# Kernel optimization log

Hardware: AMD Instinct MI355X
Metric: run time of the kernel (lower is better)

## Reference

```python
import jax, jax.numpy as jnp
import numpy as np

B, T, IDIM, HDIM = 16, 512, 80, 512
TEMPER = 10.0


def _windows(key_pad, n_shifts, win):
    idx = jnp.arange(n_shifts)[:, None] + jnp.arange(win)[None, :]
    return key_pad[..., idx]


def setup_inputs() -> dict:
    key = jax.random.key(0)
    k1, k2, k3 = jax.random.split(key, 3)
    x = jax.random.normal(k1, (B, T, IDIM), dtype=jnp.float32)
    y = jax.random.normal(k2, (B, T, IDIM), dtype=jnp.float32)
    # xavier-uniform fc1 weight, zero bias (per initialize())
    limit = float(np.sqrt(6.0 / (IDIM + HDIM)))
    fc1_w = jax.random.uniform(k3, (HDIM, IDIM), jnp.float32, -limit, limit)
    fc1_b = jnp.zeros((HDIM,), jnp.float32)
    return {"x": x, "y": y, "fc1_w": fc1_w, "fc1_b": fc1_b}


def reference(x, y, fc1_w, fc1_b):
    idim = x.shape[-1]
    pad = idim - 1                 # idim_q - 1
    S = 2 * idim - 1               # idim_k + idim_q - 1 shift positions

    # ---- _pad_for_shift: (B,T,S,idim) sliding windows over padded key ----
    key_pad = jnp.pad(x, ((0, 0), (0, 0), (pad, pad)))
    kpt = _windows(key_pad, S, idim)                        # (B,T,S,idim)

    # ---- _simiality: cosine similarity per shift, max over shifts ----
    q = y[..., None, :]                                     # (B,T,1,idim)
    denom = jnp.linalg.norm(q, axis=-1) * jnp.linalg.norm(kpt, axis=-1)
    sim = jnp.sum(q * kpt, axis=-1) / denom                 # (B,T,S)
    sim = jnp.where(jnp.isnan(sim), 0.0, sim)
    sim_max = jnp.max(sim, axis=-1)                         # (B,T)
    sim_max_idx = jnp.argmax(sim, axis=-1)                  # (B,T)

    # ---- select best-shift window (argaug, scale=False, single theta) ----
    x_aug = jnp.take_along_axis(kpt, sim_max_idx[..., None, None], axis=-2)[..., 0, :]  # (B,T,idim)

    # ---- temp_softmax attention (detached in original) ----
    score = x_aug * y
    attn = jax.nn.softmax(score / TEMPER, axis=-1)
    attn = jnp.where(jnp.isnan(attn), 0.0, attn)
    attn = jax.lax.stop_gradient(attn)
    x_attn = x_aug * attn                                   # (B,T,idim)

    # ---- _reverse_pad_for_shift: undo the shift on x_attn ----
    kp2 = jnp.pad(x_attn, ((0, 0), (0, 0), (pad, pad)))
    kpt2 = _windows(kp2, S, idim)                           # (B,T,S,idim)
    rev_idx = 2 * idim - 2 - sim_max_idx                    # p_aug = shift index
    x_ele = jnp.take_along_axis(kpt2, rev_idx[..., None, None], axis=-2)[..., 0, :]

    # ---- fc1 MLP on shifted-attended features ----
    h = jnp.einsum('bti,hi->bth', x_attn, fc1_w) + fc1_b    # (B,T,hdim)
    return h
```

## Files before the change

### kernel.cpp

```cpp
#include <hip/hip_runtime.h>
#include <math.h>

#define BT    8192
#define IDIM  80
#define HDIM  512
#define SPAN  159
#define PADX  320

__global__ __launch_bounds__(256) void k_attn(const float* __restrict__ x,
                                              const float* __restrict__ y,
                                              float* __restrict__ xattn) {
    __shared__ float xp[4][PADX];
    __shared__ float ysm[4][IDIM];
    const int w    = threadIdx.x >> 6;
    const int lane = threadIdx.x & 63;
    const int row  = blockIdx.x * 4 + w;
    const float* xr = x + (size_t)row * IDIM;
    const float* yr = y + (size_t)row * IDIM;

    for (int j = lane; j < PADX; j += 64) xp[w][j] = 0.f;
    __syncthreads();
    float yy = 0.f;
    if (lane < 20) {
        float4 xv = *(const float4*)(xr + lane * 4);
        float4 yv = *(const float4*)(yr + lane * 4);
        int b = 79 + lane * 4;
        xp[w][b + 0] = xv.x; xp[w][b + 1] = xv.y;
        xp[w][b + 2] = xv.z; xp[w][b + 3] = xv.w;
        int c = lane * 4;
        ysm[w][c + 0] = yv.x; ysm[w][c + 1] = yv.y;
        ysm[w][c + 2] = yv.z; ysm[w][c + 3] = yv.w;
        yy = yv.x * yv.x + yv.y * yv.y + yv.z * yv.z + yv.w * yv.w;
    }
    __syncthreads();
    #pragma unroll
    for (int off = 32; off; off >>= 1) yy += __shfl_xor(yy, off);

    const float* xpw = xp[w];
    const float* ysw = ysm[w];
    float d0 = 0.f, d1 = 0.f, d2 = 0.f, n0 = 0.f, n1 = 0.f, n2 = 0.f;
    #pragma unroll 4
    for (int i = 0; i < IDIM; ++i) {
        float yv = ysw[i];
        float a0 = xpw[lane + i];
        float a1 = xpw[lane + 64 + i];
        float a2 = xpw[lane + 128 + i];
        d0 += yv * a0; n0 += a0 * a0;
        d1 += yv * a1; n1 += a1 * a1;
        d2 += yv * a2; n2 += a2 * a2;
    }
    float s0 = (n0 > 0.f) ? d0 / sqrtf(yy * n0) : 0.f;
    float s1 = (n1 > 0.f) ? d1 / sqrtf(yy * n1) : 0.f;
    float s2 = (lane < 31) ? ((n2 > 0.f) ? d2 / sqrtf(yy * n2) : 0.f) : -INFINITY;

    float bv = s0; int bi = lane;
    if (s1 > bv) { bv = s1; bi = lane + 64; }
    if (s2 > bv) { bv = s2; bi = lane + 128; }
    #pragma unroll
    for (int off = 32; off; off >>= 1) {
        float ov = __shfl_xor(bv, off);
        int   oi = __shfl_xor(bi, off);
        if (ov > bv || (ov == bv && oi < bi)) { bv = ov; bi = oi; }
    }

    float xa0 = xpw[bi + lane];
    float yv0 = ysw[lane];
    float z0  = (xa0 * yv0) / 10.0f;
    float xa1 = 0.f, z1 = -INFINITY;
    if (lane < 16) {
        xa1 = xpw[bi + lane + 64];
        float yv1 = ysw[lane + 64];
        z1 = (xa1 * yv1) / 10.0f;
    }
    float m = fmaxf(z0, z1);
    #pragma unroll
    for (int off = 32; off; off >>= 1) m = fmaxf(m, __shfl_xor(m, off));
    float e0 = expf(z0 - m);
    float e1 = (lane < 16) ? expf(z1 - m) : 0.f;
    float es = e0 + e1;
    #pragma unroll
    for (int off = 32; off; off >>= 1) es += __shfl_xor(es, off);
    float inv = 1.0f / es;

    float* orow = xattn + (size_t)row * IDIM;
    orow[lane] = xa0 * (e0 * inv);
    if (lane < 16) orow[lane + 64] = xa1 * (e1 * inv);
}

__global__ __launch_bounds__(256) void k_gemm(const float* __restrict__ xattn,
                                              const float* __restrict__ wmat,
                                              const float* __restrict__ bias,
                                              float* __restrict__ out) {
    __shared__ __align__(16) float At[IDIM][64];
    __shared__ __align__(16) float Wt[IDIM][128];
    const int tid = threadIdx.x;
    const int rb  = blockIdx.x * 64;
    const int cb  = blockIdx.y * 128;

    #pragma unroll
    for (int q = 0; q < 5; ++q) {
        int idx = tid + q * 256;
        int r   = idx & 63;
        int kk  = (idx >> 6) * 4;
        float4 v = *(const float4*)(xattn + (size_t)(rb + r) * IDIM + kk);
        At[kk + 0][r] = v.x; At[kk + 1][r] = v.y;
        At[kk + 2][r] = v.z; At[kk + 3][r] = v.w;
    }
    #pragma unroll
    for (int q = 0; q < 10; ++q) {
        int idx = tid + q * 256;
        int c   = idx & 127;
        int kk  = (idx >> 7) * 4;
        float4 v = *(const float4*)(wmat + (size_t)(cb + c) * IDIM + kk);
        Wt[kk + 0][c] = v.x; Wt[kk + 1][c] = v.y;
        Wt[kk + 2][c] = v.z; Wt[kk + 3][c] = v.w;
    }
    __syncthreads();

    const int c0 = (tid & 31) * 4;
    const int r0 = (tid >> 5) * 8;
    float acc[8][4];
    #pragma unroll
    for (int r = 0; r < 8; ++r)
        #pragma unroll
        for (int c = 0; c < 4; ++c) acc[r][c] = 0.f;

    #pragma unroll 4
    for (int k = 0; k < IDIM; ++k) {
        float4 wv = *(const float4*)&Wt[k][c0];
        float4 a0 = *(const float4*)&At[k][r0];
        float4 a1 = *(const float4*)&At[k][r0 + 4];
        float a[8] = {a0.x, a0.y, a0.z, a0.w, a1.x, a1.y, a1.z, a1.w};
        #pragma unroll
        for (int r = 0; r < 8; ++r) {
            acc[r][0] += a[r] * wv.x;
            acc[r][1] += a[r] * wv.y;
            acc[r][2] += a[r] * wv.z;
            acc[r][3] += a[r] * wv.w;
        }
    }

    float4 bv = *(const float4*)(bias + cb + c0);
    #pragma unroll
    for (int r = 0; r < 8; ++r) {
        float4 o;
        o.x = acc[r][0] + bv.x;
        o.y = acc[r][1] + bv.y;
        o.z = acc[r][2] + bv.z;
        o.w = acc[r][3] + bv.w;
        *(float4*)(out + (size_t)(rb + r0 + r) * HDIM + cb + c0) = o;
    }
}

extern "C" void kernel_launch(void* const* d_in, const int* in_sizes, int n_in,
                              void* d_out, int out_size, void* d_ws, size_t ws_size,
                              hipStream_t stream) {
    const float* x  = (const float*)d_in[0];
    const float* y  = (const float*)d_in[1];
    const float* wm = (const float*)d_in[2];
    const float* bs = (const float*)d_in[3];
    float* out   = (float*)d_out;
    float* xattn = (float*)d_ws;

    k_attn<<<dim3(BT / 4), 256, 0, stream>>>(x, y, xattn);
    k_gemm<<<dim3(BT / 64, HDIM / 128), 256, 0, stream>>>(xattn, wm, bs, out);
}
```

Before: 89.93 us.

## Replace FP32 SIMT GEMM with bf16 MFMA 16x16x32 matrix-core GEMM

The fc1 projection is rewritten to convert xattn and the weights to bf16 in shared memory, zero-padding K from 80 to 96, and to compute with MFMA 16x16x32 bf16 instructions. The tile changes to 64x64 per block, with each wave handling 16 rows by 64 columns. This moves the GEMM arithmetic from scalar FMAs onto the matrix cores. In exchange it lowers input precision to bf16, which may exceed tolerance, and writes outputs as scalar strided stores instead of float4.

```diff
diff --git a/kernel.cpp b/kernel.cpp
--- a/kernel.cpp
+++ b/kernel.cpp
@@ -6,6 +6,19 @@
 #define HDIM  512
 #define SPAN  159
 #define PADX  320
+#define KPAD  96
+#define LDK   104
+
+typedef unsigned short ushort_t;
+typedef __attribute__((ext_vector_type(8))) short short8;
+typedef __attribute__((ext_vector_type(4))) float floatx4;
+typedef __attribute__((ext_vector_type(4))) unsigned short ushort4v;
+
+__device__ inline ushort_t f2bf(float f) {
+    union { float f; unsigned int i; } v; v.f = f;
+    unsigned int x = v.i;
+    return (ushort_t)((x + 0x7fffu + ((x >> 16) & 1u)) >> 16);
+}
 
 __global__ __launch_bounds__(256) void k_attn(const float* __restrict__ x,
                                               const float* __restrict__ y,
@@ -87,68 +100,66 @@
     if (lane < 16) orow[lane + 64] = xa1 * (e1 * inv);
 }
 
-__global__ __launch_bounds__(256) void k_gemm(const float* __restrict__ xattn,
-                                              const float* __restrict__ wmat,
-                                              const float* __restrict__ bias,
-                                              float* __restrict__ out) {
-    __shared__ __align__(16) float At[IDIM][64];
-    __shared__ __align__(16) float Wt[IDIM][128];
+__global__ __launch_bounds__(256) void k_gemm_mfma(const float* __restrict__ xattn,
+                                                   const float* __restrict__ wmat,
+                                                   const float* __restrict__ bias,
+                                                   float* __restrict__ out) {
+    __shared__ __align__(16) ushort_t Abf[64][LDK];
+    __shared__ __align__(16) ushort_t Wbf[64][LDK];
     const int tid = threadIdx.x;
     const int rb  = blockIdx.x * 64;
-    const int cb  = blockIdx.y * 128;
+    const int cb  = blockIdx.y * 64;
 
+    if (tid < 64) {
+        ushort4v z = {0, 0, 0, 0};
+        *(ushort4v*)&Abf[tid][80] = z; *(ushort4v*)&Abf[tid][84] = z;
+        *(ushort4v*)&Abf[tid][88] = z; *(ushort4v*)&Abf[tid][92] = z;
+        *(ushort4v*)&Wbf[tid][80] = z; *(ushort4v*)&Wbf[tid][84] = z;
+        *(ushort4v*)&Wbf[tid][88] = z; *(ushort4v*)&Wbf[tid][92] = z;
+    }
     #pragma unroll
     for (int q = 0; q < 5; ++q) {
-        int idx = tid + q * 256;
-        int r   = idx & 63;
-        int kk  = (idx >> 6) * 4;
-        float4 v = *(const float4*)(xattn + (size_t)(rb + r) * IDIM + kk);
-        At[kk + 0][r] = v.x; At[kk + 1][r] = v.y;
-        At[kk + 2][r] = v.z; At[kk + 3][r] = v.w;
-    }
-    #pragma unroll
-    for (int q = 0; q < 10; ++q) {
-        int idx = tid + q * 256;
-        int c   = idx & 127;
-        int kk  = (idx >> 7) * 4;
-        float4 v = *(const float4*)(wmat + (size_t)(cb + c) * IDIM + kk);
-        Wt[kk + 0][c] = v.x; Wt[kk + 1][c] = v.y;
-        Wt[kk + 2][c] = v.z; Wt[kk + 3][c] = v.w;
+        int idx = q * 256 + tid;
+        int r   = idx / 20;
+        int kp  = (idx % 20) * 4;
+        float4 av = *(const float4*)(xattn + (size_t)(rb + r) * IDIM + kp);
+        ushort4v ab = { f2bf(av.x), f2bf(av.y), f2bf(av.z), f2bf(av.w) };
+        *(ushort4v*)&Abf[r][kp] = ab;
+        float4 wv = *(const float4*)(wmat + (size_t)(cb + r) * IDIM + kp);
+        ushort4v wb = { f2bf(wv.x), f2bf(wv.y), f2bf(wv.z), f2bf(wv.w) };
+        *(ushort4v*)&Wbf[r][kp] = wb;
     }
     __syncthreads();
 
-    const int c0 = (tid & 31) * 4;
-    const int r0 = (tid >> 5) * 8;
-    float acc[8][4];
+    const int wv   = tid >> 6;
+    const int lane = tid & 63;
+    const int m    = lane & 15;
+    const int q4   = lane >> 4;
+
+    short8 af[3];
     #pragma unroll
-    for (int r = 0; r < 8; ++r)
+    for (int kt = 0; kt < 3; ++kt)
+        af[kt] = *(const short8*)&Abf[16 * wv + m][q4 * 8 + kt * 32];
+
+    floatx4 acc[4] = {{0.f,0.f,0.f,0.f}, {0.f,0.f,0.f,0.f},
+                      {0.f,0.f,0.f,0.f}, {0.f,0.f,0.f,0.f}};
+    #pragma unroll
+    for (int ct = 0; ct < 4; ++ct) {
         #pragma unroll
-        for (int c = 0; c < 4; ++c) acc[r][c] = 0.f;
-
-    #pragma unroll 4
-    for (int k = 0; k < IDIM; ++k) {
-        float4 wv = *(const float4*)&Wt[k][c0];
-        float4 a0 = *(const float4*)&At[k][r0];
-        float4 a1 = *(const float4*)&At[k][r0 + 4];
-        float a[8] = {a0.x, a0.y, a0.z, a0.w, a1.x, a1.y, a1.z, a1.w};
-        #pragma unroll
-        for (int r = 0; r < 8; ++r) {
-            acc[r][0] += a[r] * wv.x;
-            acc[r][1] += a[r] * wv.y;
-            acc[r][2] += a[r] * wv.z;
-            acc[r][3] += a[r] * wv.w;
+        for (int kt = 0; kt < 3; ++kt) {
+            short8 bf = *(const short8*)&Wbf[ct * 16 + m][q4 * 8 + kt * 32];
+            acc[ct] = __builtin_amdgcn_mfma_f32_16x16x32_bf16(af[kt], bf, acc[ct], 0, 0, 0);
         }
     }
 
-    float4 bv = *(const float4*)(bias + cb + c0);
     #pragma unroll
-    for (int r = 0; r < 8; ++r) {
-        float4 o;
-        o.x = acc[r][0] + bv.x;
-        o.y = acc[r][1] + bv.y;
-        o.z = acc[r][2] + bv.z;
-        o.w = acc[r][3] + bv.w;
-        *(float4*)(out + (size_t)(rb + r0 + r) * HDIM + cb + c0) = o;
+    for (int ct = 0; ct < 4; ++ct) {
+        int col = cb + ct * 16 + m;
+        float bsv = bias[col];
+        int row0 = rb + 16 * wv + q4 * 4;
+        #pragma unroll
+        for (int i = 0; i < 4; ++i)
+            out[(size_t)(row0 + i) * HDIM + col] = acc[ct][i] + bsv;
     }
 }
 
@@ -163,5 +174,5 @@
     float* xattn = (float*)d_ws;
 
     k_attn<<<dim3(BT / 4), 256, 0, stream>>>(x, y, xattn);
-    k_gemm<<<dim3(BT / 64, HDIM / 128), 256, 0, stream>>>(xattn, wm, bs, out);
+    k_gemm_mfma<<<dim3(BT / 64, HDIM / 64), 256, 0, stream>>>(xattn, wm, bs, out);
 }
```

Result: faster. 83.30 us (-7.4%).
